# Kernel optimization log

Hardware: AMD Instinct MI355X
Metric: run time of the kernel (lower is better)

## Reference

```python
import jax, jax.numpy as jnp
import numpy as np

HIDDEN = 2048
NUM_HEADS = 16
NUM_KV_HEADS = 4
HEAD_DIM = HIDDEN // NUM_HEADS  # 128
ROPE_WAVELENGTH = 1000000
ROPE_SCALING = 1.0
EPS = 1e-6


def _rotate_half(x):
    half = x.shape[-1] // 2
    return jnp.concatenate([-x[..., half:], x[..., :half]], axis=-1)


def apply_rope(x, positions, max_wavelength, scaling_factor):
    head_dim = x.shape[-1]
    inv_freq = 1.0 / max_wavelength ** (jnp.arange(0, head_dim, 2, dtype=jnp.float32) / head_dim)
    scaled_pos = positions.astype(jnp.float32) / scaling_factor
    freqs = jnp.einsum('t,d->td', scaled_pos, inv_freq)
    emb = jnp.concatenate([freqs, freqs], axis=-1)
    cos = jnp.cos(emb)[None, :, None, :]
    sin = jnp.sin(emb)[None, :, None, :]
    return x * cos + _rotate_half(x) * sin


def rms_norm(x, scale, eps=EPS):
    x32 = x.astype(jnp.float32)
    var = jnp.mean(jnp.square(x32), axis=-1, keepdims=True)
    normed = x32 * jax.lax.rsqrt(var + eps)
    return (normed * scale).astype(x.dtype)


def setup_inputs() -> dict:
    key = jax.random.key(0)
    ks = jax.random.split(key, 8)
    B, T = 2, 2048
    x = jax.random.normal(ks[0], (B, T, HIDDEN), dtype=jnp.float32)
    attention_mask = jnp.ones((B, T, T), dtype=bool)
    s = 1.0 / np.sqrt(HIDDEN)
    Wq = jax.random.normal(ks[1], (HIDDEN, NUM_HEADS, HEAD_DIM), dtype=jnp.float32) * s
    Wk = jax.random.normal(ks[2], (HIDDEN, NUM_KV_HEADS, HEAD_DIM), dtype=jnp.float32) * s
    Wv = jax.random.normal(ks[3], (HIDDEN, NUM_KV_HEADS, HEAD_DIM), dtype=jnp.float32) * s
    q_scale = jnp.ones((HEAD_DIM,), dtype=jnp.float32)
    k_scale = jnp.ones((HEAD_DIM,), dtype=jnp.float32)
    Wo = jax.random.normal(ks[4], (NUM_HEADS, HEAD_DIM, HIDDEN), dtype=jnp.float32) * (1.0 / np.sqrt(HIDDEN))
    return {"x": x, "attention_mask": attention_mask, "Wq": Wq, "Wk": Wk, "Wv": Wv,
            "q_scale": q_scale, "k_scale": k_scale, "Wo": Wo}


def reference(x, attention_mask, Wq, Wk, Wv, q_scale, k_scale, Wo):
    B, T, _ = x.shape
    q = jnp.einsum('btc,chd->bthd', x, Wq)
    k = jnp.einsum('btc,chd->bthd', x, Wk)
    v = jnp.einsum('btc,chd->bthd', x, Wv)
    q = rms_norm(q, q_scale)
    k = rms_norm(k, k_scale)
    positions = jnp.arange(T, dtype=jnp.int32)
    q = apply_rope(q, positions, ROPE_WAVELENGTH, ROPE_SCALING)
    k = apply_rope(k, positions, ROPE_WAVELENGTH, ROPE_SCALING)
    repeats = NUM_HEADS // NUM_KV_HEADS
    k = jnp.repeat(k, repeats, axis=2)
    v = jnp.repeat(v, repeats, axis=2)
    scale = HEAD_DIM ** -0.5
    attn_logits = jnp.einsum('bthd,bshd->bhts', q, k) * scale
    attn_logits = jnp.where(attention_mask[:, None, :, :], attn_logits, -1e30)
    attn = jax.nn.softmax(attn_logits.astype(jnp.float32), axis=-1).astype(x.dtype)
    attn_out = jnp.einsum('bhts,bshd->bthd', attn, v)
    return jnp.einsum('bthd,hdc->btc', attn_out, Wo)
```

## Files before the change

kernel.cpp:

```cpp
#include <hip/hip_runtime.h>

typedef __attribute__((ext_vector_type(4))) float f32x4;
typedef __attribute__((ext_vector_type(16))) float f32x16;
typedef __attribute__((ext_vector_type(8))) short short8;
typedef __attribute__((ext_vector_type(4))) unsigned short us4;
typedef __attribute__((ext_vector_type(2))) unsigned int uint2v;

#define HID 2048
#define T 2048
#define B 2
#define NH 16
#define NKV 4
#define HD 128
#define QKVN 3072

__device__ __forceinline__ unsigned short f2b(float f) {
  union { float f; unsigned u; } v; v.f = f;
  return (unsigned short)((v.u + 0x7fffu + ((v.u >> 16) & 1u)) >> 16);
}

__device__ __forceinline__ void gl_lds16(const unsigned short* g, unsigned short* l) {
  __builtin_amdgcn_global_load_lds((const __attribute__((address_space(1))) void*)g,
                                   (__attribute__((address_space(3))) void*)l, 16, 0, 0);
}

__global__ __launch_bounds__(256) void convert_x(const float* __restrict__ x,
                                                 unsigned short* __restrict__ xb) {
  size_t i = ((size_t)blockIdx.x * 256 + threadIdx.x) * 4;
  float4 v = *(const float4*)(x + i);
  us4 o;
  o.x = f2b(v.x); o.y = f2b(v.y); o.z = f2b(v.z); o.w = f2b(v.w);
  *(us4*)(xb + i) = o;
}

__global__ __launch_bounds__(256) void transpose_conv(const float* __restrict__ src,
                                                      unsigned short* __restrict__ dst,
                                                      int R, int C) {
  __shared__ float tile[32][33];
  int c0 = blockIdx.x * 32, r0 = blockIdx.y * 32;
  int tx = threadIdx.x, ty = threadIdx.y;
#pragma unroll
  for (int i = 0; i < 32; i += 8)
    tile[ty + i][tx] = src[(size_t)(r0 + ty + i) * C + c0 + tx];
  __syncthreads();
#pragma unroll
  for (int i = 0; i < 32; i += 8)
    dst[(size_t)(c0 + ty + i) * R + r0 + tx] = f2b(tile[tx][ty + i]);
}

__global__ __launch_bounds__(256) void transpose_v(const float* __restrict__ qkv,
                                                   unsigned short* __restrict__ Vt) {
  __shared__ float tile[32][33];
  int z = blockIdx.z;
  int b = z >> 2, h = z & 3;
  int t0 = blockIdx.x * 32, d0 = blockIdx.y * 32;
  int tx = threadIdx.x, ty = threadIdx.y;
  const float* src = qkv + (size_t)(b * T) * QKVN + 2560 + h * HD;
#pragma unroll
  for (int i = 0; i < 32; i += 8)
    tile[ty + i][tx] = src[(size_t)(t0 + ty + i) * QKVN + d0 + tx];
  __syncthreads();
  unsigned short* dst = Vt + (size_t)z * HD * T;
#pragma unroll
  for (int i = 0; i < 32; i += 8)
    dst[(size_t)(d0 + ty + i) * T + t0 + tx] = f2b(tile[tx][ty + i]);
}

__global__ __launch_bounds__(256) void gemm_bf16(const unsigned short* __restrict__ A,
                                                 const unsigned short* __restrict__ Bt,
                                                 float* __restrict__ C,
                                                 int M, int N, int K) {
  __shared__ unsigned short As[2][128 * 32];
  __shared__ unsigned short Bs[2][128 * 32];
  int tid = threadIdx.x;
  int wave = tid >> 6, lane = tid & 63;
  int quad = lane >> 4, l16 = lane & 15;
  int m0 = blockIdx.y * 128, n0 = blockIdx.x * 128;
  int wm = (wave >> 1) * 64, wn = (wave & 1) * 64;
  f32x4 acc[4][4] = {};

  int lrow = lane >> 2, lcol = (lane & 3) * 8;
  const unsigned short* Ag = A + (size_t)(m0 + wave * 32 + lrow) * K + lcol;
  const unsigned short* Bg = Bt + (size_t)(n0 + wave * 32 + lrow) * K + lcol;

#define GSTAGE(bb, koff)                                          \
  do {                                                            \
    gl_lds16(Ag + (koff), &As[bb][wave * 1024]);                  \
    gl_lds16(Ag + (koff) + (size_t)16 * K, &As[bb][wave * 1024 + 512]); \
    gl_lds16(Bg + (koff), &Bs[bb][wave * 1024]);                  \
    gl_lds16(Bg + (koff) + (size_t)16 * K, &Bs[bb][wave * 1024 + 512]); \
  } while (0)

  GSTAGE(0, 0);
  for (int k0 = 0; k0 < K; k0 += 32) {
    int cur = (k0 >> 5) & 1;
    __syncthreads();
    if (k0 + 32 < K) GSTAGE(cur ^ 1, k0 + 32);
    short8 a[4], b[4];
#pragma unroll
    for (int mi = 0; mi < 4; ++mi)
      a[mi] = *(short8*)(&As[cur][(wm + mi * 16 + l16) * 32 + quad * 8]);
#pragma unroll
    for (int ni = 0; ni < 4; ++ni)
      b[ni] = *(short8*)(&Bs[cur][(wn + ni * 16 + l16) * 32 + quad * 8]);
#pragma unroll
    for (int mi = 0; mi < 4; ++mi)
#pragma unroll
      for (int ni = 0; ni < 4; ++ni)
        acc[mi][ni] = __builtin_amdgcn_mfma_f32_16x16x32_bf16(a[mi], b[ni], acc[mi][ni], 0, 0, 0);
  }
#undef GSTAGE
#pragma unroll
  for (int mi = 0; mi < 4; ++mi)
#pragma unroll
    for (int r = 0; r < 4; ++r) {
      int row = m0 + wm + mi * 16 + quad * 4 + r;
      float* cp = C + (size_t)row * N + n0 + wn;
#pragma unroll
      for (int ni = 0; ni < 4; ++ni)
        cp[ni * 16 + l16] = acc[mi][ni][r];
    }
}

__global__ __launch_bounds__(256) void norm_rope(const float* __restrict__ qkv,
                                                 const float* __restrict__ q_scale,
                                                 const float* __restrict__ k_scale,
                                                 unsigned short* __restrict__ Qb,
                                                 unsigned short* __restrict__ Kb) {
  int item = blockIdx.x * 4 + (threadIdx.x >> 6);
  int lane = threadIdx.x & 63;
  int idx = item % 20;
  int bt = item / 20;
  int b = bt >> 11, t = bt & 2047;
  bool isq = idx < 16;
  int h = isq ? idx : idx - 16;
  int col = isq ? idx * HD : HID + h * HD;
  const float* src = qkv + (size_t)bt * QKVN + col;
  float x_lo = src[lane], x_hi = src[lane + 64];
  float ss = x_lo * x_lo + x_hi * x_hi;
#pragma unroll
  for (int off = 32; off > 0; off >>= 1) ss += __shfl_xor(ss, off);
  float inv = rsqrtf(ss * (1.0f / 128.0f) + 1e-6f);
  const float* sc = isq ? q_scale : k_scale;
  float nl = x_lo * inv * sc[lane];
  float nh = x_hi * inv * sc[lane + 64];
  float freq = exp2f(-(float)lane * 0.31143075889569023f);
  float ph = (float)t * freq;
  float cs = cosf(ph), sn = sinf(ph);
  float ol = nl * cs - nh * sn;
  float oh = nh * cs + nl * sn;
  if (isq) { ol *= 0.12751743f; oh *= 0.12751743f; }
  unsigned short* dst = isq ? (Qb + ((size_t)(b * NH + h) * T + t) * HD)
                            : (Kb + ((size_t)(b * NKV + h) * T + t) * HD);
  dst[lane] = f2b(ol);
  dst[lane + 64] = f2b(oh);
}

__global__ __launch_bounds__(256, 2) void attn_kernel(const unsigned short* __restrict__ Qb,
                                                      const unsigned short* __restrict__ Kb,
                                                      const unsigned short* __restrict__ Vt,
                                                      unsigned short* __restrict__ AOb) {
  __shared__ unsigned short Ks[64 * 128];
  __shared__ unsigned short Vs[128 * 64];
  __shared__ float Lred[4][32];
  int b = blockIdx.z, h = blockIdx.y;
  int t0 = blockIdx.x * 128;
  int hk = h >> 2;
  int tid = threadIdx.x, wave = tid >> 6, lane = tid & 63;
  int l31 = lane & 31, hi = lane >> 5;
  const unsigned short* Qh = Qb + (size_t)(b * NH + h) * T * HD;
  const unsigned short* Kh = Kb + (size_t)(b * NKV + hk) * T * HD;
  const unsigned short* Vh = Vt + (size_t)(b * NKV + hk) * HD * T;

  short8 qf[8];
#pragma unroll
  for (int kc = 0; kc < 8; ++kc)
    qf[kc] = *(const short8*)(Qh + (size_t)(t0 + wave * 32 + l31) * HD + kc * 16 + hi * 8);

  f32x16 o[4] = {};
  float l_r = 0.0f;

  int krow4 = tid >> 4, kc4 = tid & 15;
  int kphys = (kc4 ^ (krow4 & 7)) * 8;
  int vrow8 = tid >> 3, vc8 = tid & 7;
  int vphys = (vc8 ^ (vrow8 & 7)) * 8;

  short8 kreg[4], vreg[4];
#pragma unroll
  for (int i = 0; i < 4; ++i) {
    kreg[i] = *(const short8*)(Kh + (size_t)(i * 16 + krow4) * HD + kc4 * 8);
    vreg[i] = *(const short8*)(Vh + (size_t)(i * 32 + vrow8) * T + vc8 * 8);
  }

  int swk = l31 & 7;
  for (int s0 = 0; s0 < T; s0 += 64) {
#pragma unroll
    for (int i = 0; i < 4; ++i) {
      *(short8*)(&Ks[(i * 16 + krow4) * 128 + kphys]) = kreg[i];
      *(short8*)(&Vs[(i * 32 + vrow8) * 64 + vphys]) = vreg[i];
    }
    __syncthreads();
    if (s0 + 64 < T) {
#pragma unroll
      for (int i = 0; i < 4; ++i) {
        kreg[i] = *(const short8*)(Kh + (size_t)(s0 + 64 + i * 16 + krow4) * HD + kc4 * 8);
        vreg[i] = *(const short8*)(Vh + (size_t)(i * 32 + vrow8) * T + s0 + 64 + vc8 * 8);
      }
    }
    f32x16 st[2] = {};
    __builtin_amdgcn_s_setprio(1);
#pragma unroll
    for (int kc = 0; kc < 8; ++kc) {
#pragma unroll
      for (int n = 0; n < 2; ++n) {
        short8 ka = *(short8*)(&Ks[(n * 32 + l31) * 128 + (((2 * kc + hi) ^ swk) * 8)]);
        st[n] = __builtin_amdgcn_mfma_f32_32x32x16_bf16(ka, qf[kc], st[n], 0, 0, 0);
      }
    }
    __builtin_amdgcn_s_setprio(0);
    unsigned pw0[2][4], pw1[2][4];
#pragma unroll
    for (int n = 0; n < 2; ++n)
#pragma unroll
      for (int c = 0; c < 4; ++c) {
        float p0 = exp2f(st[n][c * 4 + 0] - 17.0f);
        float p1 = exp2f(st[n][c * 4 + 1] - 17.0f);
        float p2 = exp2f(st[n][c * 4 + 2] - 17.0f);
        float p3 = exp2f(st[n][c * 4 + 3] - 17.0f);
        l_r += (p0 + p1) + (p2 + p3);
        asm("v_cvt_pk_bf16_f32 %0, %1, %2" : "=v"(pw0[n][c]) : "v"(p0), "v"(p1));
        asm("v_cvt_pk_bf16_f32 %0, %1, %2" : "=v"(pw1[n][c]) : "v"(p2), "v"(p3));
      }
    __builtin_amdgcn_s_setprio(1);
#pragma unroll
    for (int ks = 0; ks < 4; ++ks) {
      int n = ks >> 1, ce = (ks & 1) * 2;
      uint2v r0 = __builtin_amdgcn_permlane32_swap(pw0[n][ce], pw0[n][ce + 1], false, false);
      uint2v r1 = __builtin_amdgcn_permlane32_swap(pw1[n][ce], pw1[n][ce + 1], false, false);
      union { unsigned u[4]; short8 s; } pu;
      pu.u[0] = r0[0]; pu.u[1] = r1[0]; pu.u[2] = r0[1]; pu.u[3] = r1[1];
#pragma unroll
      for (int df = 0; df < 4; ++df) {
        short8 vf = *(short8*)(&Vs[(df * 32 + l31) * 64 + (((2 * ks + hi) ^ swk) * 8)]);
        o[df] = __builtin_amdgcn_mfma_f32_32x32x16_bf16(pu.s, vf, o[df], 0, 0, 0);
      }
    }
    __builtin_amdgcn_s_setprio(0);
    __syncthreads();
  }

  float lt = l_r + __shfl_xor(l_r, 32);
  if (hi == 0) Lred[wave][l31] = 1.0f / lt;
  float linv[16];
#pragma unroll
  for (int reg = 0; reg < 16; ++reg)
    linv[reg] = Lred[wave][(reg & 3) + 8 * (reg >> 2) + 4 * hi];
  int tb = t0 + wave * 32;
#pragma unroll
  for (int df = 0; df < 4; ++df)
#pragma unroll
    for (int reg = 0; reg < 16; ++reg) {
      int q = (reg & 3) + 8 * (reg >> 2) + 4 * hi;
      AOb[((size_t)(b * T) + tb + q) * HID + h * HD + df * 32 + l31] = f2b(o[df][reg] * linv[reg]);
    }
}

extern "C" void kernel_launch(void* const* d_in, const int* in_sizes, int n_in,
                              void* d_out, int out_size, void* d_ws, size_t ws_size,
                              hipStream_t stream) {
  const float* x = (const float*)d_in[0];
  const float* Wq = (const float*)d_in[2];
  const float* Wk = (const float*)d_in[3];
  const float* Wv = (const float*)d_in[4];
  const float* q_scale = (const float*)d_in[5];
  const float* k_scale = (const float*)d_in[6];
  const float* Wo = (const float*)d_in[7];
  float* out = (float*)d_out;

  char* ws = (char*)d_ws;
  const size_t MB = 1024 * 1024;
  float* qkv_f32 = (float*)(ws + 0);
  unsigned short* xb  = (unsigned short*)(ws + 48 * MB);
  unsigned short* AOb = xb;
  unsigned short* Wb  = (unsigned short*)(ws + 64 * MB);
  unsigned short* Wob = (unsigned short*)(ws + 76 * MB);
  unsigned short* Qb  = (unsigned short*)(ws + 84 * MB);
  unsigned short* Kb  = (unsigned short*)(ws + 100 * MB);
  unsigned short* Vtg = (unsigned short*)(ws + 104 * MB);

  dim3 tb32(32, 8);
  convert_x<<<(B * T * HID) / 1024, 256, 0, stream>>>(x, xb);
  transpose_conv<<<dim3(64, 64), tb32, 0, stream>>>(Wq, Wb, HID, 2048);
  transpose_conv<<<dim3(16, 64), tb32, 0, stream>>>(Wk, Wb + (size_t)2048 * HID, HID, 512);
  transpose_conv<<<dim3(16, 64), tb32, 0, stream>>>(Wv, Wb + (size_t)2560 * HID, HID, 512);
  transpose_conv<<<dim3(64, 64), tb32, 0, stream>>>(Wo, Wob, HID, 2048);
  gemm_bf16<<<dim3(QKVN / 128, (B * T) / 128), 256, 0, stream>>>(xb, Wb, qkv_f32, B * T, QKVN, HID);
  norm_rope<<<(B * T * 20) / 4, 256, 0, stream>>>(qkv_f32, q_scale, k_scale, Qb, Kb);
  transpose_v<<<dim3(T / 32, HD / 32, B * NKV), tb32, 0, stream>>>(qkv_f32, Vtg);
  attn_kernel<<<dim3(T / 128, NH, B), 256, 0, stream>>>(Qb, Kb, Vtg, AOb);
  gemm_bf16<<<dim3(HID / 128, (B * T) / 128), 256, 0, stream>>>(AOb, Wob, out, B * T, HID, HID);
}
```

Measured before the change: 365.7 us.

## Merge preprocessing launches and double-buffer K/V tiles in attention

```diff
diff --git a/kernel.cpp b/kernel.cpp
--- a/kernel.cpp
+++ b/kernel.cpp
@@ -33,11 +33,22 @@
   *(us4*)(xb + i) = o;
 }
 
-__global__ __launch_bounds__(256) void transpose_conv(const float* __restrict__ src,
-                                                      unsigned short* __restrict__ dst,
-                                                      int R, int C) {
+__global__ __launch_bounds__(256) void transpose_all(const float* __restrict__ Wq,
+                                                     const float* __restrict__ Wk,
+                                                     const float* __restrict__ Wv,
+                                                     const float* __restrict__ Wo,
+                                                     unsigned short* __restrict__ Wb,
+                                                     unsigned short* __restrict__ Wob) {
   __shared__ float tile[32][33];
-  int c0 = blockIdx.x * 32, r0 = blockIdx.y * 32;
+  int bx = blockIdx.x;
+  const float* src;
+  unsigned short* dst;
+  int C, cx;
+  if (bx < 64)      { src = Wq; dst = Wb;                        C = 2048; cx = bx; }
+  else if (bx < 80) { src = Wk; dst = Wb + (size_t)2048 * HID;   C = 512;  cx = bx - 64; }
+  else if (bx < 96) { src = Wv; dst = Wb + (size_t)2560 * HID;   C = 512;  cx = bx - 80; }
+  else              { src = Wo; dst = Wob;                       C = 2048; cx = bx - 96; }
+  int c0 = cx * 32, r0 = blockIdx.y * 32;
   int tx = threadIdx.x, ty = threadIdx.y;
 #pragma unroll
   for (int i = 0; i < 32; i += 8)
@@ -45,25 +56,7 @@
   __syncthreads();
 #pragma unroll
   for (int i = 0; i < 32; i += 8)
-    dst[(size_t)(c0 + ty + i) * R + r0 + tx] = f2b(tile[tx][ty + i]);
-}
-
-__global__ __launch_bounds__(256) void transpose_v(const float* __restrict__ qkv,
-                                                   unsigned short* __restrict__ Vt) {
-  __shared__ float tile[32][33];
-  int z = blockIdx.z;
-  int b = z >> 2, h = z & 3;
-  int t0 = blockIdx.x * 32, d0 = blockIdx.y * 32;
-  int tx = threadIdx.x, ty = threadIdx.y;
-  const float* src = qkv + (size_t)(b * T) * QKVN + 2560 + h * HD;
-#pragma unroll
-  for (int i = 0; i < 32; i += 8)
-    tile[ty + i][tx] = src[(size_t)(t0 + ty + i) * QKVN + d0 + tx];
-  __syncthreads();
-  unsigned short* dst = Vt + (size_t)z * HD * T;
-#pragma unroll
-  for (int i = 0; i < 32; i += 8)
-    dst[(size_t)(d0 + ty + i) * T + t0 + tx] = f2b(tile[tx][ty + i]);
+    dst[(size_t)(c0 + ty + i) * HID + r0 + tx] = f2b(tile[tx][ty + i]);
 }
 
 __global__ __launch_bounds__(256) void gemm_bf16(const unsigned short* __restrict__ A,
@@ -122,46 +115,67 @@
     }
 }
 
-__global__ __launch_bounds__(256) void norm_rope(const float* __restrict__ qkv,
-                                                 const float* __restrict__ q_scale,
-                                                 const float* __restrict__ k_scale,
-                                                 unsigned short* __restrict__ Qb,
-                                                 unsigned short* __restrict__ Kb) {
-  int item = blockIdx.x * 4 + (threadIdx.x >> 6);
-  int lane = threadIdx.x & 63;
-  int idx = item % 20;
-  int bt = item / 20;
-  int b = bt >> 11, t = bt & 2047;
-  bool isq = idx < 16;
-  int h = isq ? idx : idx - 16;
-  int col = isq ? idx * HD : HID + h * HD;
-  const float* src = qkv + (size_t)bt * QKVN + col;
-  float x_lo = src[lane], x_hi = src[lane + 64];
-  float ss = x_lo * x_lo + x_hi * x_hi;
-#pragma unroll
-  for (int off = 32; off > 0; off >>= 1) ss += __shfl_xor(ss, off);
-  float inv = rsqrtf(ss * (1.0f / 128.0f) + 1e-6f);
-  const float* sc = isq ? q_scale : k_scale;
-  float nl = x_lo * inv * sc[lane];
-  float nh = x_hi * inv * sc[lane + 64];
-  float freq = exp2f(-(float)lane * 0.31143075889569023f);
-  float ph = (float)t * freq;
-  float cs = cosf(ph), sn = sinf(ph);
-  float ol = nl * cs - nh * sn;
-  float oh = nh * cs + nl * sn;
-  if (isq) { ol *= 0.12751743f; oh *= 0.12751743f; }
-  unsigned short* dst = isq ? (Qb + ((size_t)(b * NH + h) * T + t) * HD)
-                            : (Kb + ((size_t)(b * NKV + h) * T + t) * HD);
-  dst[lane] = f2b(ol);
-  dst[lane + 64] = f2b(oh);
+__global__ __launch_bounds__(256) void norm_fused(const float* __restrict__ qkv,
+                                                  const float* __restrict__ q_scale,
+                                                  const float* __restrict__ k_scale,
+                                                  unsigned short* __restrict__ Qb,
+                                                  unsigned short* __restrict__ Kb,
+                                                  unsigned short* __restrict__ Vt) {
+  __shared__ float tile[32][33];
+  if (blockIdx.x < 20480) {
+    int item = blockIdx.x * 4 + (threadIdx.x >> 6);
+    int lane = threadIdx.x & 63;
+    int idx = item % 20;
+    int bt = item / 20;
+    int b = bt >> 11, t = bt & 2047;
+    bool isq = idx < 16;
+    int h = isq ? idx : idx - 16;
+    int col = isq ? idx * HD : HID + h * HD;
+    const float* src = qkv + (size_t)bt * QKVN + col;
+    float x_lo = src[lane], x_hi = src[lane + 64];
+    float ss = x_lo * x_lo + x_hi * x_hi;
+#pragma unroll
+    for (int off = 32; off > 0; off >>= 1) ss += __shfl_xor(ss, off);
+    float inv = rsqrtf(ss * (1.0f / 128.0f) + 1e-6f);
+    const float* sc = isq ? q_scale : k_scale;
+    float nl = x_lo * inv * sc[lane];
+    float nh = x_hi * inv * sc[lane + 64];
+    float freq = exp2f(-(float)lane * 0.31143075889569023f);
+    float ph = (float)t * freq;
+    float cs = cosf(ph), sn = sinf(ph);
+    float ol = nl * cs - nh * sn;
+    float oh = nh * cs + nl * sn;
+    if (isq) { ol *= 0.12751743f; oh *= 0.12751743f; }
+    unsigned short* dst = isq ? (Qb + ((size_t)(b * NH + h) * T + t) * HD)
+                              : (Kb + ((size_t)(b * NKV + h) * T + t) * HD);
+    dst[lane] = f2b(ol);
+    dst[lane + 64] = f2b(oh);
+  } else {
+    int zi = blockIdx.x - 20480;
+    int z = zi >> 8;
+    int rem = zi & 255;
+    int d0 = (rem >> 6) * 32;
+    int t0 = (rem & 63) * 32;
+    int b = z >> 2, h = z & 3;
+    int tx = threadIdx.x & 31, ty = threadIdx.x >> 5;
+    const float* src = qkv + (size_t)(b * T) * QKVN + 2560 + h * HD;
+#pragma unroll
+    for (int i = 0; i < 32; i += 8)
+      tile[ty + i][tx] = src[(size_t)(t0 + ty + i) * QKVN + d0 + tx];
+    __syncthreads();
+    unsigned short* dst = Vt + (size_t)z * HD * T;
+#pragma unroll
+    for (int i = 0; i < 32; i += 8)
+      dst[(size_t)(d0 + ty + i) * T + t0 + tx] = f2b(tile[tx][ty + i]);
+  }
 }
 
 __global__ __launch_bounds__(256, 2) void attn_kernel(const unsigned short* __restrict__ Qb,
                                                       const unsigned short* __restrict__ Kb,
                                                       const unsigned short* __restrict__ Vt,
                                                       unsigned short* __restrict__ AOb) {
-  __shared__ unsigned short Ks[64 * 128];
-  __shared__ unsigned short Vs[128 * 64];
+  __shared__ unsigned short Ks[2][64 * 128];
+  __shared__ unsigned short Vs[2][128 * 64];
   __shared__ float Lred[4][32];
   int b = blockIdx.z, h = blockIdx.y;
   int t0 = blockIdx.x * 128;
@@ -191,20 +205,36 @@
     kreg[i] = *(const short8*)(Kh + (size_t)(i * 16 + krow4) * HD + kc4 * 8);
     vreg[i] = *(const short8*)(Vh + (size_t)(i * 32 + vrow8) * T + vc8 * 8);
   }
+#pragma unroll
+  for (int i = 0; i < 4; ++i) {
+    *(short8*)(&Ks[0][(i * 16 + krow4) * 128 + kphys]) = kreg[i];
+    *(short8*)(&Vs[0][(i * 32 + vrow8) * 64 + vphys]) = vreg[i];
+  }
+#pragma unroll
+  for (int i = 0; i < 4; ++i) {
+    kreg[i] = *(const short8*)(Kh + (size_t)(64 + i * 16 + krow4) * HD + kc4 * 8);
+    vreg[i] = *(const short8*)(Vh + (size_t)(i * 32 + vrow8) * T + 64 + vc8 * 8);
+  }
+  __syncthreads();
 
   int swk = l31 & 7;
-  for (int s0 = 0; s0 < T; s0 += 64) {
-#pragma unroll
-    for (int i = 0; i < 4; ++i) {
-      *(short8*)(&Ks[(i * 16 + krow4) * 128 + kphys]) = kreg[i];
-      *(short8*)(&Vs[(i * 32 + vrow8) * 64 + vphys]) = vreg[i];
-    }
-    __syncthreads();
-    if (s0 + 64 < T) {
+  for (int n = 0; n < 32; ++n) {
+    int cur = n & 1;
+    const unsigned short* Kw = Ks[cur];
+    const unsigned short* Vw = Vs[cur];
+    if (n + 1 < 32) {
 #pragma unroll
       for (int i = 0; i < 4; ++i) {
-        kreg[i] = *(const short8*)(Kh + (size_t)(s0 + 64 + i * 16 + krow4) * HD + kc4 * 8);
-        vreg[i] = *(const short8*)(Vh + (size_t)(i * 32 + vrow8) * T + s0 + 64 + vc8 * 8);
+        *(short8*)(&Ks[cur ^ 1][(i * 16 + krow4) * 128 + kphys]) = kreg[i];
+        *(short8*)(&Vs[cur ^ 1][(i * 32 + vrow8) * 64 + vphys]) = vreg[i];
+      }
+    }
+    if (n + 2 < 32) {
+      int s2 = (n + 2) * 64;
+#pragma unroll
+      for (int i = 0; i < 4; ++i) {
+        kreg[i] = *(const short8*)(Kh + (size_t)(s2 + i * 16 + krow4) * HD + kc4 * 8);
+        vreg[i] = *(const short8*)(Vh + (size_t)(i * 32 + vrow8) * T + s2 + vc8 * 8);
       }
     }
     f32x16 st[2] = {};
@@ -212,36 +242,36 @@
 #pragma unroll
     for (int kc = 0; kc < 8; ++kc) {
 #pragma unroll
-      for (int n = 0; n < 2; ++n) {
-        short8 ka = *(short8*)(&Ks[(n * 32 + l31) * 128 + (((2 * kc + hi) ^ swk) * 8)]);
-        st[n] = __builtin_amdgcn_mfma_f32_32x32x16_bf16(ka, qf[kc], st[n], 0, 0, 0);
+      for (int nn = 0; nn < 2; ++nn) {
+        short8 ka = *(short8*)(&Kw[(nn * 32 + l31) * 128 + (((2 * kc + hi) ^ swk) * 8)]);
+        st[nn] = __builtin_amdgcn_mfma_f32_32x32x16_bf16(ka, qf[kc], st[nn], 0, 0, 0);
       }
     }
     __builtin_amdgcn_s_setprio(0);
     unsigned pw0[2][4], pw1[2][4];
 #pragma unroll
-    for (int n = 0; n < 2; ++n)
+    for (int nn = 0; nn < 2; ++nn)
 #pragma unroll
       for (int c = 0; c < 4; ++c) {
-        float p0 = exp2f(st[n][c * 4 + 0] - 17.0f);
-        float p1 = exp2f(st[n][c * 4 + 1] - 17.0f);
-        float p2 = exp2f(st[n][c * 4 + 2] - 17.0f);
-        float p3 = exp2f(st[n][c * 4 + 3] - 17.0f);
+        float p0 = exp2f(st[nn][c * 4 + 0] - 17.0f);
+        float p1 = exp2f(st[nn][c * 4 + 1] - 17.0f);
+        float p2 = exp2f(st[nn][c * 4 + 2] - 17.0f);
+        float p3 = exp2f(st[nn][c * 4 + 3] - 17.0f);
         l_r += (p0 + p1) + (p2 + p3);
-        asm("v_cvt_pk_bf16_f32 %0, %1, %2" : "=v"(pw0[n][c]) : "v"(p0), "v"(p1));
-        asm("v_cvt_pk_bf16_f32 %0, %1, %2" : "=v"(pw1[n][c]) : "v"(p2), "v"(p3));
+        asm("v_cvt_pk_bf16_f32 %0, %1, %2" : "=v"(pw0[nn][c]) : "v"(p0), "v"(p1));
+        asm("v_cvt_pk_bf16_f32 %0, %1, %2" : "=v"(pw1[nn][c]) : "v"(p2), "v"(p3));
       }
     __builtin_amdgcn_s_setprio(1);
 #pragma unroll
     for (int ks = 0; ks < 4; ++ks) {
-      int n = ks >> 1, ce = (ks & 1) * 2;
-      uint2v r0 = __builtin_amdgcn_permlane32_swap(pw0[n][ce], pw0[n][ce + 1], false, false);
-      uint2v r1 = __builtin_amdgcn_permlane32_swap(pw1[n][ce], pw1[n][ce + 1], false, false);
+      int nn = ks >> 1, ce = (ks & 1) * 2;
+      uint2v r0 = __builtin_amdgcn_permlane32_swap(pw0[nn][ce], pw0[nn][ce + 1], false, false);
+      uint2v r1 = __builtin_amdgcn_permlane32_swap(pw1[nn][ce], pw1[nn][ce + 1], false, false);
       union { unsigned u[4]; short8 s; } pu;
       pu.u[0] = r0[0]; pu.u[1] = r1[0]; pu.u[2] = r0[1]; pu.u[3] = r1[1];
 #pragma unroll
       for (int df = 0; df < 4; ++df) {
-        short8 vf = *(short8*)(&Vs[(df * 32 + l31) * 64 + (((2 * ks + hi) ^ swk) * 8)]);
+        short8 vf = *(short8*)(&Vw[(df * 32 + l31) * 64 + (((2 * ks + hi) ^ swk) * 8)]);
         o[df] = __builtin_amdgcn_mfma_f32_32x32x16_bf16(pu.s, vf, o[df], 0, 0, 0);
       }
     }
@@ -290,13 +320,9 @@
 
   dim3 tb32(32, 8);
   convert_x<<<(B * T * HID) / 1024, 256, 0, stream>>>(x, xb);
-  transpose_conv<<<dim3(64, 64), tb32, 0, stream>>>(Wq, Wb, HID, 2048);
-  transpose_conv<<<dim3(16, 64), tb32, 0, stream>>>(Wk, Wb + (size_t)2048 * HID, HID, 512);
-  transpose_conv<<<dim3(16, 64), tb32, 0, stream>>>(Wv, Wb + (size_t)2560 * HID, HID, 512);
-  transpose_conv<<<dim3(64, 64), tb32, 0, stream>>>(Wo, Wob, HID, 2048);
+  transpose_all<<<dim3(160, 64), tb32, 0, stream>>>(Wq, Wk, Wv, Wo, Wb, Wob);
   gemm_bf16<<<dim3(QKVN / 128, (B * T) / 128), 256, 0, stream>>>(xb, Wb, qkv_f32, B * T, QKVN, HID);
-  norm_rope<<<(B * T * 20) / 4, 256, 0, stream>>>(qkv_f32, q_scale, k_scale, Qb, Kb);
-  transpose_v<<<dim3(T / 32, HD / 32, B * NKV), tb32, 0, stream>>>(qkv_f32, Vtg);
+  norm_fused<<<20480 + 2048, 256, 0, stream>>>(qkv_f32, q_scale, k_scale, Qb, Kb, Vtg);
   attn_kernel<<<dim3(T / 128, NH, B), 256, 0, stream>>>(Qb, Kb, Vtg, AOb);
   gemm_bf16<<<dim3(HID / 128, (B * T) / 128), 256, 0, stream>>>(AOb, Wob, out, B * T, HID, HID);
 }
```

New measurement: 357.3 us. 2.3% less time.
